# Kernel optimization log

Hardware: AMD Instinct MI355X
Metric: run time of the kernel (lower is better)

The kernel has to match this reference:

```python
import jax, jax.numpy as jnp
import numpy as np


def setup_inputs() -> dict:
    key = jax.random.key(0)
    ks = jax.random.split(key, 5)
    B, I, H = 16384, 1024, 1024
    return {
        "input": jax.random.normal(ks[0], (B, I), dtype=jnp.float32),
        "h_prev": jax.random.normal(ks[1], (B, H), dtype=jnp.float32),
        "c_prev": jax.random.normal(ks[2], (B, H), dtype=jnp.float32),
        "W_ih": jax.random.normal(ks[3], (4 * H, I), dtype=jnp.float32),
        "W_hh": jax.random.normal(ks[4], (4 * H, H), dtype=jnp.float32),
        "b_ih": jnp.zeros((4 * H,), dtype=jnp.float32),
        "b_hh": jnp.zeros((4 * H,), dtype=jnp.float32),
    }


def reference(input, h_prev, c_prev, W_ih, W_hh, b_ih, b_hh):
    H = h_prev.shape[1]
    gi = input @ W_ih.T + b_ih          # [B, 4H]
    gh = h_prev @ W_hh.T + b_hh         # [B, 4H]
    g = gi + gh
    # chunk order in source: input_gate, forget_gate, candidate, output_gate
    i_g = jax.nn.sigmoid(g[:, 0 * H:1 * H])
    f_g = jax.nn.sigmoid(g[:, 1 * H:2 * H])
    cand = jnp.tanh(g[:, 2 * H:3 * H])
    o_g = jax.nn.sigmoid(g[:, 3 * H:4 * H])
    c_new = c_prev * f_g + i_g * cand
    h_new = jnp.tanh(c_new) * o_g
    return (h_new, c_new)
```

## Files before the change

kernel.cpp:

```cpp
#include <hip/hip_runtime.h>
#include <cstdint>
#include <cstddef>


typedef _Float16 half8 __attribute__((ext_vector_type(8)));
typedef float f32x4 __attribute__((ext_vector_type(4)));

__device__ __forceinline__ float sigmoidf_(float x) { return 1.0f / (1.0f + __expf(-x)); }
__device__ __forceinline__ float tanh_fast(float x) { return 2.0f / (1.0f + __expf(-2.0f * x)) - 1.0f; }

__device__ __forceinline__ void gld16(const void* g, void* lds) {
    __builtin_amdgcn_global_load_lds((const __attribute__((address_space(1))) uint32_t*)g,
                                     (__attribute__((address_space(3))) uint32_t*)lds, 16, 0, 0);
}

__global__ __launch_bounds__(256)
void convert_to_f16(const float* __restrict__ X, const float* __restrict__ H,
                    const float* __restrict__ Wih, const float* __restrict__ Whh,
                    _Float16* __restrict__ ws, long nX, long nW)
{
    long e = ((long)blockIdx.x * 256 + threadIdx.x) * 8;
    long total = 2 * nX + 2 * nW;
    if (e >= total) return;
    const float* src; long off;
    if (e < nX)              { src = X;   off = e; }
    else if (e < 2 * nX)     { src = H;   off = e - nX; }
    else if (e < 2 * nX + nW){ src = Wih; off = e - 2 * nX; }
    else                     { src = Whh; off = e - 2 * nX - nW; }
    float4 a = *(const float4*)(src + off);
    float4 b = *(const float4*)(src + off + 4);
    half8 h;
    h[0]=(_Float16)a.x; h[1]=(_Float16)a.y; h[2]=(_Float16)a.z; h[3]=(_Float16)a.w;
    h[4]=(_Float16)b.x; h[5]=(_Float16)b.y; h[6]=(_Float16)b.z; h[7]=(_Float16)b.w;
    *(half8*)(ws + e) = h;
}

__global__ __launch_bounds__(512, 2)
void lstm_mfma_v6(const _Float16* __restrict__ ws,
                  const float* __restrict__ Cprev,
                  const float* __restrict__ bih, const float* __restrict__ bhh,
                  float* __restrict__ Out, int Btot, int mblocks)
{
    __shared__ alignas(16) char smem[131072];

    const long nX = (long)Btot * 1024;
    const long nW = 4096L * 1024;
    const _Float16* Xh = ws;
    const _Float16* Hh = ws + nX;
    const _Float16* Wi = ws + 2 * nX;
    const _Float16* Wh = ws + 2 * nX + nW;

    const int tid = threadIdx.x;
    const int w = tid >> 6, l = tid & 63;
    const int lr = l & 15, q = l >> 4;
    const int wm = w >> 2, wn = w & 3;

    const int nwg = gridDim.x;
    int bx = blockIdx.x;
    if ((nwg & 7) == 0) bx = (bx & 7) * (nwg >> 3) + (bx >> 3);
    const int hblk = (bx & 15) * 64;
    const int m0   = (bx >> 4) * 256;

    uint32_t gA[2], gB[2], ub[2];
    #pragma unroll
    for (int j = 0; j < 2; ++j) {
        uint32_t u = (uint32_t)(j * 8192 + w * 1024);
        ub[j] = u;
        uint32_t off = u + (uint32_t)l * 16u;
        uint32_t r  = off >> 6;
        uint32_t c  = ((off >> 4) & 3u) ^ ((r >> 1) & 3u);
        gA[j] = (uint32_t)(m0 + (int)r) * 1024u + c * 8u;
        uint32_t gate = (r >> 4) & 3u;
        uint32_t hsub = (r >> 6) * 16u + (r & 15u);
        gB[j] = (gate * 1024u + (uint32_t)hblk + hsub) * 1024u + c * 8u;
    }

    const int sw = (lr >> 1) & 3;
    const int ck = (q ^ sw) * 16;
    const char* adA = smem + (uint32_t)((wm * 128 + lr) * 64 + ck);
    const char* adB = smem + 65536u + (uint32_t)((wn * 64 + lr) * 64 + ck);

    f32x4 acc[8][4];
    #pragma unroll
    for (int i = 0; i < 8; ++i)
        #pragma unroll
        for (int j = 0; j < 4; ++j)
            acc[i][j] = (f32x4){0.f, 0.f, 0.f, 0.f};

    auto stageA = [&](int ts, int sb) {
        const _Float16* Ap = (ts < 32) ? Xh : Hh;
        const uint32_t k0 = (uint32_t)(ts & 31) * 32u;
        char* bA = smem + sb * 16384;
        gld16(Ap + gA[0] + k0, bA + ub[0]);
        gld16(Ap + gA[1] + k0, bA + ub[1]);
    };
    auto stageB = [&](int ts, int sb) {
        const _Float16* Bp = (ts < 32) ? Wi : Wh;
        const uint32_t k0 = (uint32_t)(ts & 31) * 32u;
        char* bB = smem + 65536 + sb * 16384;
        gld16(Bp + gB[0] + k0, bB + ub[0]);
        gld16(Bp + gB[1] + k0, bB + ub[1]);
    };

    stageA(0, 0); stageB(0, 0);
    stageA(1, 1); stageB(1, 1);
    stageA(2, 2); stageB(2, 2);
    asm volatile("s_waitcnt vmcnt(8)" ::: "memory");
    __builtin_amdgcn_s_barrier();

#define TILE(T, SLOT)                                                                \
    {                                                                                \
        int ts_ = (T) + 3; if (ts_ > 63) ts_ = 63;                                   \
        const int sb_ = ((T) + 3) & 3;                                               \
        half8 af[4], bf[4], ag[4];                                                   \
        _Pragma("unroll")                                                            \
        for (int i = 0; i < 4; ++i) bf[i] = *(const half8*)(adB + (SLOT) * 16384 + i * 1024); \
        _Pragma("unroll")                                                            \
        for (int i = 0; i < 4; ++i) af[i] = *(const half8*)(adA + (SLOT) * 16384 + i * 1024); \
        stageA(ts_, sb_);                                                            \
        __builtin_amdgcn_s_barrier();                                                \
        asm volatile("s_waitcnt lgkmcnt(0)" ::: "memory");                           \
        __builtin_amdgcn_s_setprio(1);                                               \
        _Pragma("unroll")                                                            \
        for (int mt = 0; mt < 4; ++mt)                                               \
            _Pragma("unroll")                                                        \
            for (int nt = 0; nt < 4; ++nt)                                           \
                acc[mt][nt] = __builtin_amdgcn_mfma_f32_16x16x32_f16(af[mt], bf[nt], acc[mt][nt], 0, 0, 0); \
        __builtin_amdgcn_s_setprio(0);                                               \
        __builtin_amdgcn_s_barrier();                                                \
        _Pragma("unroll")                                                            \
        for (int i = 0; i < 4; ++i) ag[i] = *(const half8*)(adA + (SLOT) * 16384 + (i + 4) * 1024); \
        stageB(ts_, sb_);                                                            \
        __builtin_amdgcn_s_barrier();                                                \
        asm volatile("s_waitcnt lgkmcnt(0)" ::: "memory");                           \
        __builtin_amdgcn_s_setprio(1);                                               \
        _Pragma("unroll")                                                            \
        for (int mt = 0; mt < 4; ++mt)                                               \
            _Pragma("unroll")                                                        \
            for (int nt = 0; nt < 4; ++nt)                                           \
                acc[mt + 4][nt] = __builtin_amdgcn_mfma_f32_16x16x32_f16(ag[mt], bf[nt], acc[mt + 4][nt], 0, 0, 0); \
        __builtin_amdgcn_s_setprio(0);                                               \
        asm volatile("s_waitcnt vmcnt(8)" ::: "memory");                             \
        __builtin_amdgcn_s_barrier();                                                \
    }

    #pragma unroll 1
    for (int p = 0; p < 16; ++p) {
        TILE(4 * p + 0, 0)
        TILE(4 * p + 1, 1)
        TILE(4 * p + 2, 2)
        TILE(4 * p + 3, 3)
    }
#undef TILE
    asm volatile("s_waitcnt vmcnt(0)" ::: "memory");

    const int h = hblk + wn * 16 + lr;
    float bs[4];
    #pragma unroll
    for (int g = 0; g < 4; ++g) bs[g] = bih[g * 1024 + h] + bhh[g * 1024 + h];
    const long c_off = (long)Btot * 1024;
    const int mbase = m0 + wm * 128 + q * 4;

    #pragma unroll
    for (int mt = 0; mt < 8; ++mt) {
        #pragma unroll
        for (int r = 0; r < 4; ++r) {
            const int m = mbase + mt * 16 + r;
            const long idx = (long)m * 1024 + h;
            float gi = acc[mt][0][r] + bs[0];
            float gf = acc[mt][1][r] + bs[1];
            float gc = acc[mt][2][r] + bs[2];
            float go = acc[mt][3][r] + bs[3];
            float ig = sigmoidf_(gi), fg = sigmoidf_(gf);
            float cd = tanh_fast(gc), og = sigmoidf_(go);
            float c_new = Cprev[idx] * fg + ig * cd;
            Out[idx]         = tanh_fast(c_new) * og;
            Out[c_off + idx] = c_new;
        }
    }
}

__global__ __launch_bounds__(256, 2)
void lstm_mfma_f16_fb(const float* __restrict__ X, const float* __restrict__ Hprev,
                      const float* __restrict__ Cprev,
                      const float* __restrict__ Wih, const float* __restrict__ Whh,
                      const float* __restrict__ bih, const float* __restrict__ bhh,
                      float* __restrict__ Out, int Btot, int mblocks)
{
    __shared__ alignas(16) _Float16 As[128][40];
    __shared__ alignas(16) _Float16 Bs[256][40];
    const int tid = threadIdx.x;
    const int w = tid >> 6, lane = tid & 63, lr = lane & 15, q = lane >> 4;
    const int bx = blockIdx.x, mblk = bx % mblocks, nblk = bx / mblocks;
    const int m0 = mblk * 128, hblk = nblk * 64;
    const int sr = tid >> 1, sc = tid & 1;
    f32x4 acc[8][4];
    #pragma unroll
    for (int mt = 0; mt < 8; ++mt)
        #pragma unroll
        for (int g = 0; g < 4; ++g) acc[mt][g] = (f32x4){0.f,0.f,0.f,0.f};
    float4 pa[4], pb0[4], pb1[4];
    const int rb1 = sr + 128;
    const size_t wrow0 = (size_t)((sr >> 6) * 1024 + hblk + (sr & 63)) * 1024;
    const size_t wrow1 = (size_t)((rb1 >> 6) * 1024 + hblk + (rb1 & 63)) * 1024;
    const size_t arow  = (size_t)(m0 + sr) * 1024;
    auto stage_load = [&](int tile) {
        const int phase = tile >> 5;
        const int k0 = (tile & 31) * 32 + sc * 16;
        const float* Ap = phase ? Hprev : X;
        const float* Wp = phase ? Whh : Wih;
        const float4* ap = (const float4*)(Ap + arow + k0);
        const float4* b0 = (const float4*)(Wp + wrow0 + k0);
        const float4* b1 = (const float4*)(Wp + wrow1 + k0);
        #pragma unroll
        for (int i = 0; i < 4; ++i) { pa[i] = ap[i]; pb0[i] = b0[i]; pb1[i] = b1[i]; }
    };
    auto pack8 = [](float4 a, float4 b) {
        half8 h;
        h[0]=(_Float16)a.x; h[1]=(_Float16)a.y; h[2]=(_Float16)a.z; h[3]=(_Float16)a.w;
        h[4]=(_Float16)b.x; h[5]=(_Float16)b.y; h[6]=(_Float16)b.z; h[7]=(_Float16)b.w;
        return h;
    };
    stage_load(0);
    for (int tile = 0; tile < 64; ++tile) {
        __syncthreads();
        *(half8*)&As[sr][sc*16]        = pack8(pa[0], pa[1]);
        *(half8*)&As[sr][sc*16+8]      = pack8(pa[2], pa[3]);
        *(half8*)&Bs[sr][sc*16]        = pack8(pb0[0], pb0[1]);
        *(half8*)&Bs[sr][sc*16+8]      = pack8(pb0[2], pb0[3]);
        *(half8*)&Bs[sr+128][sc*16]    = pack8(pb1[0], pb1[1]);
        *(half8*)&Bs[sr+128][sc*16+8]  = pack8(pb1[2], pb1[3]);
        __syncthreads();
        if (tile + 1 < 64) stage_load(tile + 1);
        half8 bf[4];
        #pragma unroll
        for (int g = 0; g < 4; ++g) bf[g] = *(const half8*)&Bs[g*64 + w*16 + lr][q*8];
        #pragma unroll
        for (int mt = 0; mt < 8; ++mt) {
            half8 a = *(const half8*)&As[mt*16 + lr][q*8];
            #pragma unroll
            for (int g = 0; g < 4; ++g)
                acc[mt][g] = __builtin_amdgcn_mfma_f32_16x16x32_f16(a, bf[g], acc[mt][g], 0, 0, 0);
        }
    }
    const int h = hblk + w * 16 + lr;
    float bs0 = bih[h] + bhh[h];
    float bs1 = bih[1024+h] + bhh[1024+h];
    float bs2 = bih[2048+h] + bhh[2048+h];
    float bs3 = bih[3072+h] + bhh[3072+h];
    const size_t c_off = (size_t)Btot * 1024;
    #pragma unroll
    for (int mt = 0; mt < 8; ++mt)
        #pragma unroll
        for (int r = 0; r < 4; ++r) {
            const int m = m0 + mt*16 + q*4 + r;
            const size_t idx = (size_t)m * 1024 + h;
            float gi = acc[mt][0][r]+bs0, gf = acc[mt][1][r]+bs1;
            float gc = acc[mt][2][r]+bs2, go = acc[mt][3][r]+bs3;
            float ig = sigmoidf_(gi), fg = sigmoidf_(gf);
            float cd = tanh_fast(gc), og = sigmoidf_(go);
            float c_new = Cprev[idx]*fg + ig*cd;
            Out[idx] = tanh_fast(c_new)*og;
            Out[c_off+idx] = c_new;
        }
}

extern "C" void kernel_launch(void* const* d_in, const int* in_sizes, int n_in,
                              void* d_out, int out_size, void* d_ws, size_t ws_size,
                              hipStream_t stream) {
    const float* X     = (const float*)d_in[0];
    const float* Hprev = (const float*)d_in[1];
    const float* Cprev = (const float*)d_in[2];
    const float* Wih   = (const float*)d_in[3];
    const float* Whh   = (const float*)d_in[4];
    const float* bih   = (const float*)d_in[5];
    const float* bhh   = (const float*)d_in[6];
    float* Out = (float*)d_out;

    const int Btot = in_sizes[0] / 1024;
    const long nX = (long)Btot * 1024, nW = 4096L * 1024;
    const size_t need = (size_t)(2 * nX + 2 * nW) * sizeof(_Float16);

    if (ws_size >= need && (Btot % 256) == 0) {
        _Float16* ws = (_Float16*)d_ws;
        const long total = 2 * nX + 2 * nW;
        const int cblocks = (int)((total / 8 + 255) / 256);
        hipLaunchKernelGGL(convert_to_f16, dim3(cblocks), dim3(256), 0, stream,
                           X, Hprev, Wih, Whh, ws, nX, nW);
        const int mblocks = Btot / 256;
        const int nblocks = 1024 / 64;
        hipLaunchKernelGGL(lstm_mfma_v6, dim3(mblocks * nblocks), dim3(512), 0, stream,
                           ws, Cprev, bih, bhh, Out, Btot, mblocks);
    } else {
        const int mblocks = Btot / 128;
        hipLaunchKernelGGL(lstm_mfma_f16_fb, dim3(mblocks * 16), dim3(256), 0, stream,
                           X, Hprev, Cprev, Wih, Whh, bih, bhh, Out, Btot, mblocks);
    }
}
```

Baseline: 553.2 us.

## Widen K-tile to 64 with double-buffered halves and finer phase pipeline

Restructures the MFMA main loop so each LDS stage holds K=64 (128-byte rows with an XOR swizzle over 8 chunks) instead of K=32, with two buffers split into half-tiles. Each tile is processed in eight phases over quadrants of M and N, and each phase issues one half-tile global-to-LDS load. This halves the number of K iterations and barriers per unit of work and aims to overlap loads with MFMA more evenly. In exchange, prefetch depth drops from three tiles ahead to roughly one, which may expose memory latency, and the wait counts have to match the load ordering exactly.

```diff
diff --git a/kernel.cpp b/kernel.cpp
--- a/kernel.cpp
+++ b/kernel.cpp
@@ -36,7 +36,7 @@
 }
 
 __global__ __launch_bounds__(512, 2)
-void lstm_mfma_v6(const _Float16* __restrict__ ws,
+void lstm_mfma_v7(const _Float16* __restrict__ ws,
                   const float* __restrict__ Cprev,
                   const float* __restrict__ bih, const float* __restrict__ bhh,
                   float* __restrict__ Out, int Btot, int mblocks)
@@ -61,97 +61,99 @@
     const int hblk = (bx & 15) * 64;
     const int m0   = (bx >> 4) * 256;
 
-    uint32_t gA[2], gB[2], ub[2];
+    uint32_t gA0[2], gB0[2];
     #pragma unroll
     for (int j = 0; j < 2; ++j) {
-        uint32_t u = (uint32_t)(j * 8192 + w * 1024);
-        ub[j] = u;
-        uint32_t off = u + (uint32_t)l * 16u;
-        uint32_t r  = off >> 6;
-        uint32_t c  = ((off >> 4) & 3u) ^ ((r >> 1) & 3u);
-        gA[j] = (uint32_t)(m0 + (int)r) * 1024u + c * 8u;
-        uint32_t gate = (r >> 4) & 3u;
-        uint32_t hsub = (r >> 6) * 16u + (r & 15u);
-        gB[j] = (gate * 1024u + (uint32_t)hblk + hsub) * 1024u + c * 8u;
-    }
-
-    const int sw = (lr >> 1) & 3;
-    const int ck = (q ^ sw) * 16;
-    const char* adA = smem + (uint32_t)((wm * 128 + lr) * 64 + ck);
-    const char* adB = smem + 65536u + (uint32_t)((wn * 64 + lr) * 64 + ck);
+        uint32_t off = (uint32_t)(j * 8192 + w * 1024 + l * 16);
+        uint32_t lr_ = off >> 7;
+        uint32_t cl  = (off >> 4) & 7u;
+        uint32_t cg  = cl ^ (lr_ & 7u);
+        gA0[j] = (uint32_t)(m0 + (int)lr_) * 1024u + cg * 8u;
+        uint32_t g_  = (lr_ >> 4) & 3u;
+        uint32_t hs  = (lr_ >> 6) * 16u + (lr_ & 15u);
+        gB0[j] = (g_ * 1024u + (uint32_t)hblk + hs) * 1024u + cg * 8u;
+    }
+    const uint32_t ub0 = (uint32_t)(w * 1024);
+    const uint32_t ub1 = (uint32_t)(8192 + w * 1024);
+
+    const uint32_t ckA0 = (uint32_t)(((0 * 4 + q) ^ (lr & 7)) * 16);
+    const uint32_t ckA1 = (uint32_t)(((1 * 4 + q) ^ (lr & 7)) * 16);
+    const char* pA0 = smem + (uint32_t)((wm * 128 + lr) * 128) + ckA0;
+    const char* pA1 = smem + (uint32_t)((wm * 128 + lr) * 128) + ckA1;
+    const char* pB0 = smem + 65536u + (uint32_t)((wn * 64 + lr) * 128) + ckA0;
+    const char* pB1 = smem + 65536u + (uint32_t)((wn * 64 + lr) * 128) + ckA1;
 
     f32x4 acc[8][4];
     #pragma unroll
     for (int i = 0; i < 8; ++i)
         #pragma unroll
-        for (int j = 0; j < 4; ++j)
-            acc[i][j] = (f32x4){0.f, 0.f, 0.f, 0.f};
-
-    auto stageA = [&](int ts, int sb) {
-        const _Float16* Ap = (ts < 32) ? Xh : Hh;
-        const uint32_t k0 = (uint32_t)(ts & 31) * 32u;
-        char* bA = smem + sb * 16384;
-        gld16(Ap + gA[0] + k0, bA + ub[0]);
-        gld16(Ap + gA[1] + k0, bA + ub[1]);
+        for (int jj = 0; jj < 4; ++jj)
+            acc[i][jj] = (f32x4){0.f, 0.f, 0.f, 0.f};
+
+    auto stage = [&](int which, int bufsel, int h, int ts) {
+        const _Float16* src;
+        uint32_t g0, g1;
+        if (which == 0) { src = (ts < 16) ? Xh : Hh; g0 = gA0[0] + (uint32_t)h * 131072u; g1 = gA0[1] + (uint32_t)h * 131072u; }
+        else            { src = (ts < 16) ? Wi : Wh; g0 = gB0[0] + (uint32_t)h * 32768u;  g1 = gB0[1] + (uint32_t)h * 32768u;  }
+        const uint32_t kof = (uint32_t)(ts & 15) * 64u;
+        char* base = smem + (which ? 65536 : 0) + bufsel * 32768 + h * 16384;
+        gld16(src + g0 + kof, base + ub0);
+        gld16(src + g1 + kof, base + ub1);
     };
-    auto stageB = [&](int ts, int sb) {
-        const _Float16* Bp = (ts < 32) ? Wi : Wh;
-        const uint32_t k0 = (uint32_t)(ts & 31) * 32u;
-        char* bB = smem + 65536 + sb * 16384;
-        gld16(Bp + gB[0] + k0, bB + ub[0]);
-        gld16(Bp + gB[1] + k0, bB + ub[1]);
-    };
-
-    stageA(0, 0); stageB(0, 0);
-    stageA(1, 1); stageB(1, 1);
-    stageA(2, 2); stageB(2, 2);
-    asm volatile("s_waitcnt vmcnt(8)" ::: "memory");
+
+    half8 af[4][2], bf[2][2];
+
+    stage(0, 0, 0, 0); stage(0, 0, 1, 0);
+    stage(1, 0, 0, 0); stage(1, 0, 1, 0);
+    stage(0, 1, 0, 1);
+    asm volatile("s_waitcnt vmcnt(2)" ::: "memory");
     __builtin_amdgcn_s_barrier();
 
-#define TILE(T, SLOT)                                                                \
+#define PH(BUFSEL, MQ, NQ, READA, SW, SB, SH, ST, DOVM)                              \
     {                                                                                \
-        int ts_ = (T) + 3; if (ts_ > 63) ts_ = 63;                                   \
-        const int sb_ = ((T) + 3) & 3;                                               \
-        half8 af[4], bf[4], ag[4];                                                   \
+        if (READA) {                                                                 \
+            _Pragma("unroll")                                                        \
+            for (int mt = 0; mt < 4; ++mt) {                                         \
+                af[mt][0] = *(const half8*)(pA0 + (BUFSEL) * 32768 + (MQ) * 8192 + mt * 2048); \
+                af[mt][1] = *(const half8*)(pA1 + (BUFSEL) * 32768 + (MQ) * 8192 + mt * 2048); \
+            }                                                                        \
+        }                                                                            \
         _Pragma("unroll")                                                            \
-        for (int i = 0; i < 4; ++i) bf[i] = *(const half8*)(adB + (SLOT) * 16384 + i * 1024); \
-        _Pragma("unroll")                                                            \
-        for (int i = 0; i < 4; ++i) af[i] = *(const half8*)(adA + (SLOT) * 16384 + i * 1024); \
-        stageA(ts_, sb_);                                                            \
+        for (int gl = 0; gl < 2; ++gl) {                                             \
+            bf[gl][0] = *(const half8*)(pB0 + (BUFSEL) * 32768 + ((NQ) * 2 + gl) * 2048); \
+            bf[gl][1] = *(const half8*)(pB1 + (BUFSEL) * 32768 + ((NQ) * 2 + gl) * 2048); \
+        }                                                                            \
+        stage((SW), (SB), (SH), (ST));                                               \
         __builtin_amdgcn_s_barrier();                                                \
         asm volatile("s_waitcnt lgkmcnt(0)" ::: "memory");                           \
         __builtin_amdgcn_s_setprio(1);                                               \
         _Pragma("unroll")                                                            \
         for (int mt = 0; mt < 4; ++mt)                                               \
             _Pragma("unroll")                                                        \
-            for (int nt = 0; nt < 4; ++nt)                                           \
-                acc[mt][nt] = __builtin_amdgcn_mfma_f32_16x16x32_f16(af[mt], bf[nt], acc[mt][nt], 0, 0, 0); \
+            for (int gl = 0; gl < 2; ++gl) {                                         \
+                acc[(MQ)*4+mt][(NQ)*2+gl] = __builtin_amdgcn_mfma_f32_16x16x32_f16(af[mt][0], bf[gl][0], acc[(MQ)*4+mt][(NQ)*2+gl], 0, 0, 0); \
+                acc[(MQ)*4+mt][(NQ)*2+gl] = __builtin_amdgcn_mfma_f32_16x16x32_f16(af[mt][1], bf[gl][1], acc[(MQ)*4+mt][(NQ)*2+gl], 0, 0, 0); \
+            }                                                                        \
         __builtin_amdgcn_s_setprio(0);                                               \
+        if (DOVM) asm volatile("s_waitcnt vmcnt(2)" ::: "memory");                   \
         __builtin_amdgcn_s_barrier();                                                \
-        _Pragma("unroll")                                                            \
-        for (int i = 0; i < 4; ++i) ag[i] = *(const half8*)(adA + (SLOT) * 16384 + (i + 4) * 1024); \
-        stageB(ts_, sb_);                                                            \
-        __builtin_amdgcn_s_barrier();                                                \
-        asm volatile("s_waitcnt lgkmcnt(0)" ::: "memory");                           \
-        __builtin_amdgcn_s_setprio(1);                                               \
-        _Pragma("unroll")                                                            \
-        for (int mt = 0; mt < 4; ++mt)                                               \
-            _Pragma("unroll")                                                        \
-            for (int nt = 0; nt < 4; ++nt)                                           \
-                acc[mt + 4][nt] = __builtin_amdgcn_mfma_f32_16x16x32_f16(ag[mt], bf[nt], acc[mt + 4][nt], 0, 0, 0); \
-        __builtin_amdgcn_s_setprio(0);                                               \
-        asm volatile("s_waitcnt vmcnt(8)" ::: "memory");                             \
-        __builtin_amdgcn_s_barrier();                                                \
     }
 
     #pragma unroll 1
-    for (int p = 0; p < 16; ++p) {
-        TILE(4 * p + 0, 0)
-        TILE(4 * p + 1, 1)
-        TILE(4 * p + 2, 2)
-        TILE(4 * p + 3, 3)
-    }
-#undef TILE
+    for (int j = 0; j < 16; ++j) {
+        const int t1 = 2 * j + 1;
+        const int tp = (2 * j + 2 > 31) ? 31 : 2 * j + 2;
+        const int tq = (2 * j + 3 > 31) ? 31 : 2 * j + 3;
+        PH(0, 0, 0, 1, 0, 1, 1, t1, 0)
+        PH(0, 0, 1, 0, 1, 1, 0, t1, 0)
+        PH(0, 1, 0, 1, 1, 1, 1, t1, 0)
+        PH(0, 1, 1, 0, 0, 0, 0, tp, 1)
+        PH(1, 0, 0, 1, 0, 0, 1, tp, 0)
+        PH(1, 0, 1, 0, 1, 0, 0, tp, 0)
+        PH(1, 1, 0, 1, 1, 0, 1, tp, 0)
+        PH(1, 1, 1, 0, 0, 1, 0, tq, 1)
+    }
+#undef PH
     asm volatile("s_waitcnt vmcnt(0)" ::: "memory");
 
     const int h = hblk + wn * 16 + lr;
@@ -162,15 +164,15 @@
     const int mbase = m0 + wm * 128 + q * 4;
 
     #pragma unroll
-    for (int mt = 0; mt < 8; ++mt) {
+    for (int mf = 0; mf < 8; ++mf) {
         #pragma unroll
         for (int r = 0; r < 4; ++r) {
-            const int m = mbase + mt * 16 + r;
+            const int m = mbase + mf * 16 + r;
             const long idx = (long)m * 1024 + h;
-            float gi = acc[mt][0][r] + bs[0];
-            float gf = acc[mt][1][r] + bs[1];
-            float gc = acc[mt][2][r] + bs[2];
-            float go = acc[mt][3][r] + bs[3];
+            float gi = acc[mf][0][r] + bs[0];
+            float gf = acc[mf][1][r] + bs[1];
+            float gc = acc[mf][2][r] + bs[2];
+            float go = acc[mf][3][r] + bs[3];
             float ig = sigmoidf_(gi), fg = sigmoidf_(gf);
             float cd = tanh_fast(gc), og = sigmoidf_(go);
             float c_new = Cprev[idx] * fg + ig * cd;
@@ -289,7 +291,7 @@
                            X, Hprev, Wih, Whh, ws, nX, nW);
         const int mblocks = Btot / 256;
         const int nblocks = 1024 / 64;
-        hipLaunchKernelGGL(lstm_mfma_v6, dim3(mblocks * nblocks), dim3(512), 0, stream,
+        hipLaunchKernelGGL(lstm_mfma_v7, dim3(mblocks * nblocks), dim3(512), 0, stream,
                            ws, Cprev, bih, bhh, Out, Btot, mblocks);
     } else {
         const int mblocks = Btot / 128;
```

Result: slower. 570.8 us (+3.2%).
